# Kernel tuning notes

Hardware: AMD Instinct MI355X
Metric: run time of the kernel (lower is better)

The kernel has to match this reference:

```python
import jax, jax.numpy as jnp
import numpy as np
from jax import lax

B, C, L = 32, 64, 16384
C_OUT = 64


def conv1d(x, w, b):
    # x: [B,C,L], w: [Cout,Cin,K], b: [Cout]
    y = lax.conv_general_dilated(x, w, window_strides=(1,), padding='VALID',
                                 dimension_numbers=('NCH', 'OIH', 'NCH'))
    return y + b[None, :, None]


def setup_inputs() -> dict:
    key = jax.random.key(0)
    k1, k2, k3, k4, k5 = jax.random.split(key, 5)
    x = jax.random.normal(k1, (B, C, L), dtype=jnp.float32)
    # kernel_size = 1 (see shape_source); PyTorch Conv1d default init scale ~ 1/sqrt(Cin*K)
    s = 1.0 / np.sqrt(C * 1)
    offset_w = jax.random.uniform(k2, (C * 1, C, 1), jnp.float32, -s, s)
    offset_b = jax.random.uniform(k3, (C * 1,), jnp.float32, -s, s)
    regular_w = jax.random.uniform(k4, (C_OUT, C, 1), jnp.float32, -s, s)
    regular_b = jax.random.uniform(k5, (C_OUT,), jnp.float32, -s, s)
    return {'x': x, 'offset_w': offset_w, 'offset_b': offset_b,
            'regular_w': regular_w, 'regular_b': regular_b}


def reference(x, offset_w, offset_b, regular_w, regular_b):
    Bx, Cx, Lx = x.shape
    offsets = conv1d(x, offset_w, offset_b)                 # [B,C,L]
    base = jnp.arange(Lx, dtype=x.dtype)[None, None, :]      # [1,1,L]
    indices = jnp.clip(base + offsets, 0.0, Lx - 1)          # [B,C,L] float positions
    idx_floor = jnp.floor(indices)
    idx_ceil = jnp.ceil(indices)
    x_floor = jnp.take_along_axis(x, idx_floor.astype(jnp.int32), axis=2)
    x_ceil = jnp.take_along_axis(x, idx_ceil.astype(jnp.int32), axis=2)
    frac = indices - idx_floor
    x_deform = (1.0 - frac) * x_floor + frac * x_ceil        # [B,C,L]
    return conv1d(x_deform, regular_w, regular_b)            # [B,Cout,L]
```

## Files before the change

### kernel.cpp

```cpp
#include <hip/hip_runtime.h>


#define BDIM 256
#define BB   32
#define CC   64
#define LL   16384
#define TL   64
#define HH   8
#define ROWS (TL + 2*HH)
#define RSW  36
#define XGS  82

typedef __fp16 half_t;
typedef __attribute__((ext_vector_type(2))) __fp16 h2;
typedef __attribute__((ext_vector_type(8))) __fp16 h8;
typedef __attribute__((ext_vector_type(4))) float f4;

union H2U { h2 h; unsigned u; };
union H8U { unsigned u[4]; h8 v; };

static __device__ __forceinline__ unsigned pk(float a, float b) {
    H2U r; r.h = __builtin_amdgcn_cvt_pkrtz(a, b); return r.u;
}

static __device__ __forceinline__ void load_a_split(const float* __restrict__ wp,
                                                    int row, int ks, int q,
                                                    h8* ahi, h8* alo) {
    const float* base = wp + row * 64 + ks * 32 + q * 8;
    float4 w0 = *(const float4*)base;
    float4 w1 = *(const float4*)(base + 4);
    float v[8] = {w0.x, w0.y, w0.z, w0.w, w1.x, w1.y, w1.z, w1.w};
    H8U h, l;
    #pragma unroll
    for (int p = 0; p < 4; ++p) {
        H2U hh; hh.h = __builtin_amdgcn_cvt_pkrtz(v[2*p], v[2*p+1]);
        h.u[p] = hh.u;
        l.u[p] = pk(v[2*p] - (float)hh.h[0], v[2*p+1] - (float)hh.h[1]);
    }
    *ahi = h.v; *alo = l.v;
}

static __device__ __forceinline__ h8 load_a_f16(const float* __restrict__ wp,
                                                int row, int ks, int q) {
    const float* base = wp + row * 64 + ks * 32 + q * 8;
    float4 w0 = *(const float4*)base;
    float4 w1 = *(const float4*)(base + 4);
    float v[8] = {w0.x, w0.y, w0.z, w0.w, w1.x, w1.y, w1.z, w1.w};
    H8U r;
    #pragma unroll
    for (int p = 0; p < 4; ++p) r.u[p] = pk(v[2*p], v[2*p+1]);
    return r.v;
}

__global__ __launch_bounds__(BDIM)
void deform_conv1d_r4(const float* __restrict__ x,
                      const float* __restrict__ offw,
                      const float* __restrict__ offb,
                      const float* __restrict__ regw,
                      const float* __restrict__ regb,
                      float* __restrict__ out) {
    __shared__ __align__(16) unsigned char smem[9216 + 9216 + 10496];
    unsigned* XtH = (unsigned*)smem;
    unsigned* XtL = (unsigned*)(smem + 9216);
    half_t*   Xg  = (half_t*)(smem + 18432);
    unsigned* XdW = (unsigned*)smem;

    const int tid = threadIdx.x;
    const int bx  = blockIdx.x;
    const int lg0 = bx * TL;
    const int b   = blockIdx.y;
    const size_t xb = (size_t)b * CC * LL;

    if (bx >= 1 && bx <= (LL / TL) - 2) {
        for (int i = tid; i < 320; i += BDIM) {
            int cb = i / 20, lb = i - cb * 20;
            int c0 = cb * 4;
            int l0 = lg0 - HH + lb * 4;
            const float* pp = x + xb + (size_t)c0 * LL + l0;
            float4 v0 = *(const float4*)(pp);
            float4 v1 = *(const float4*)(pp + LL);
            float4 v2 = *(const float4*)(pp + 2 * LL);
            float4 v3 = *(const float4*)(pp + 3 * LL);
            unsigned* gw = (unsigned*)Xg;
            int wi = 41 * c0 + 2 * lb;
            gw[wi]       = pk(v0.x, v0.y); gw[wi + 1]   = pk(v0.z, v0.w);
            gw[wi + 41]  = pk(v1.x, v1.y); gw[wi + 42]  = pk(v1.z, v1.w);
            gw[wi + 82]  = pk(v2.x, v2.y); gw[wi + 83]  = pk(v2.z, v2.w);
            gw[wi + 123] = pk(v3.x, v3.y); gw[wi + 124] = pk(v3.z, v3.w);
            if (lb >= 2 && lb < 18) {
                int m = lb - 2;
                float e0[4] = {v0.x, v0.y, v0.z, v0.w};
                float e1[4] = {v1.x, v1.y, v1.z, v1.w};
                float e2[4] = {v2.x, v2.y, v2.z, v2.w};
                float e3[4] = {v3.x, v3.y, v3.z, v3.w};
                int blkw  = (cb >> 1) ^ (m & 7);
                int wbase = (4 * m) * RSW + (blkw << 2) + 2 * (cb & 1);
                #pragma unroll
                for (int rl = 0; rl < 4; ++rl) {
                    float a = e0[rl], bb = e1[rl], cc = e2[rl], dd = e3[rl];
                    H2U h0, h1;
                    h0.h = __builtin_amdgcn_cvt_pkrtz(a, bb);
                    h1.h = __builtin_amdgcn_cvt_pkrtz(cc, dd);
                    int widx = wbase + rl * RSW;
                    uint2 hw; hw.x = h0.u; hw.y = h1.u;
                    *(uint2*)&XtH[widx] = hw;
                    uint2 lw;
                    lw.x = pk(a  - (float)h0.h[0], bb - (float)h0.h[1]);
                    lw.y = pk(cc - (float)h1.h[0], dd - (float)h1.h[1]);
                    *(uint2*)&XtL[widx] = lw;
                }
            }
        }
    } else {
        for (int i = tid; i < ROWS * CC; i += BDIM) {
            int r = i >> 6, c = i & 63;
            int g = min(max(lg0 - HH + r, 0), LL - 1);
            float v = x[xb + (size_t)c * LL + g];
            H2U hv; hv.h = __builtin_amdgcn_cvt_pkrtz(v, 0.0f);
            Xg[c * XGS + r] = hv.h[0];
            int row = r - HH;
            if (row >= 0 && row < TL) {
                int blkw = (c >> 3) ^ ((row >> 2) & 7);
                int widx = row * RSW + (blkw << 2) + ((c >> 1) & 3);
                float lo = v - (float)hv.h[0];
                H2U lv; lv.h = __builtin_amdgcn_cvt_pkrtz(lo, 0.0f);
                ((half_t*)XtH)[2 * widx + (c & 1)] = hv.h[0];
                ((half_t*)XtL)[2 * widx + (c & 1)] = lv.h[0];
            }
        }
    }

    const int wv   = tid >> 6;
    const int lane = tid & 63;
    const int q    = lane >> 4;
    const int n    = lane & 15;

    h8 ahi[2], alo[2];
    load_a_split(offw, 16 * wv + n, 0, q, &ahi[0], &alo[0]);
    load_a_split(offw, 16 * wv + n, 1, q, &ahi[1], &alo[1]);
    f4 acc[4];
    {
        float4 bo = *(const float4*)(offb + 16 * wv + 4 * q);
        #pragma unroll
        for (int nt = 0; nt < 4; ++nt) acc[nt] = (f4){bo.x, bo.y, bo.z, bo.w};
    }
    __syncthreads();

    #pragma unroll
    for (int nt = 0; nt < 4; ++nt) {
        const int row = 16 * nt + n;
        const int rb  = row * RSW;
        const int sb  = (row >> 2) & 7;
        #pragma unroll
        for (int ks = 0; ks < 2; ++ks) {
            int blk = (4 * ks + q) ^ sb;
            h8 bh = *(const h8*)&XtH[rb + (blk << 2)];
            h8 bl = *(const h8*)&XtL[rb + (blk << 2)];
            acc[nt] = __builtin_amdgcn_mfma_f32_16x16x32_f16(ahi[ks], bh, acc[nt], 0, 0, 0);
            acc[nt] = __builtin_amdgcn_mfma_f32_16x16x32_f16(ahi[ks], bl, acc[nt], 0, 0, 0);
            acc[nt] = __builtin_amdgcn_mfma_f32_16x16x32_f16(alo[ks], bh, acc[nt], 0, 0, 0);
        }
    }

    #pragma unroll
    for (int nt = 0; nt < 4; ++nt) {
        const int l = lg0 + 16 * nt + n;
        #pragma unroll
        for (int reg = 0; reg < 4; ++reg) {
            const int c = 16 * wv + 4 * q + reg;
            float o  = acc[nt][reg];
            float p  = (float)l + o;
            p = __builtin_amdgcn_fmed3f(p, 0.0f, (float)(LL - 1));
            float of = floorf(p);
            float fr = p - of;
            int idx  = (int)of;
            int u    = idx - lg0 + HH;
            float x0, x1;
            if ((unsigned)u <= (unsigned)(ROWS - 2)) {
                const half_t* gp = Xg + c * XGS + u;
                x0 = (float)gp[0];
                x1 = (float)gp[1];
            } else {
                const float* xr = x + xb + (size_t)c * LL;
                x0 = xr[idx];
                x1 = xr[idx + (fr > 0.0f ? 1 : 0)];
            }
            acc[nt][reg] = x0 + fr * (x1 - x0);
        }
    }

    __syncthreads();

    #pragma unroll
    for (int nt = 0; nt < 4; ++nt) {
        const int row = 16 * nt + n;
        const int sb  = (row >> 2) & 7;
        const int bw  = (2 * wv + (q >> 1)) ^ sb;
        uint2 pw;
        pw.x = pk(acc[nt][0], acc[nt][1]);
        pw.y = pk(acc[nt][2], acc[nt][3]);
        *(uint2*)&XdW[row * RSW + (bw << 2) + 2 * (q & 1)] = pw;
    }

    h8 a2[2];
    a2[0] = load_a_f16(regw, 16 * wv + n, 0, q);
    a2[1] = load_a_f16(regw, 16 * wv + n, 1, q);
    {
        float4 br = *(const float4*)(regb + 16 * wv + 4 * q);
        #pragma unroll
        for (int nt = 0; nt < 4; ++nt) acc[nt] = (f4){br.x, br.y, br.z, br.w};
    }
    __syncthreads();

    #pragma unroll
    for (int nt = 0; nt < 4; ++nt) {
        const int row = 16 * nt + n;
        const int sb  = (row >> 2) & 7;
        #pragma unroll
        for (int ks = 0; ks < 2; ++ks) {
            int blk = (4 * ks + q) ^ sb;
            h8 bv = *(const h8*)&XdW[row * RSW + (blk << 2)];
            acc[nt] = __builtin_amdgcn_mfma_f32_16x16x32_f16(a2[ks], bv, acc[nt], 0, 0, 0);
        }
    }

    float* op = out + (size_t)b * CC * LL;
    #pragma unroll
    for (int nt = 0; nt < 4; ++nt) {
        #pragma unroll
        for (int reg = 0; reg < 4; ++reg) {
            op[(size_t)(16 * wv + 4 * q + reg) * LL + lg0 + 16 * nt + n] = acc[nt][reg];
        }
    }
}

extern "C" void kernel_launch(void* const* d_in, const int* in_sizes, int n_in,
                              void* d_out, int out_size, void* d_ws, size_t ws_size,
                              hipStream_t stream) {
    const float* x    = (const float*)d_in[0];
    const float* offw = (const float*)d_in[1];
    const float* offb = (const float*)d_in[2];
    const float* regw = (const float*)d_in[3];
    const float* regb = (const float*)d_in[4];
    float* out = (float*)d_out;

    dim3 grid(LL / TL, BB);
    deform_conv1d_r4<<<grid, dim3(BDIM), 0, stream>>>(x, offw, offb, regw, regb, out);
}
```

Before: 271.6 us.

## Merge gather tile into transposed fp16 tile, drop x-lo split and barrier

Removes the separate channel-major fp16 gather buffer and the low-part x split. One swizzled row-major fp16 tile with a halo now serves both the offset MFMA B operand and the bilinear gather, and the halo shrinks from 8 to 4. This cuts the offset GEMM from three MFMAs to two per step, reduces LDS footprint and staging stores, and removes a __syncthreads because the deformed output now goes to a separate region. In exchange, x is rounded to fp16 in the offset conv, which may hurt offset accuracy, and more gathers fall back to global memory because the halo is smaller.

```diff
diff --git a/kernel.cpp b/kernel.cpp
--- a/kernel.cpp
+++ b/kernel.cpp
@@ -6,10 +6,10 @@
 #define CC   64
 #define LL   16384
 #define TL   64
-#define HH   8
+#define HH   4
 #define ROWS (TL + 2*HH)
 #define RSW  36
-#define XGS  82
+#define RSH  72
 
 typedef __fp16 half_t;
 typedef __attribute__((ext_vector_type(2))) __fp16 h2;
@@ -53,17 +53,18 @@
 }
 
 __global__ __launch_bounds__(BDIM)
-void deform_conv1d_r4(const float* __restrict__ x,
+void deform_conv1d_r5(const float* __restrict__ x,
                       const float* __restrict__ offw,
                       const float* __restrict__ offb,
                       const float* __restrict__ regw,
                       const float* __restrict__ regb,
                       float* __restrict__ out) {
-    __shared__ __align__(16) unsigned char smem[9216 + 9216 + 10496];
+    __shared__ __align__(16) unsigned char smem[10368 + 9216];
     unsigned* XtH = (unsigned*)smem;
-    unsigned* XtL = (unsigned*)(smem + 9216);
-    half_t*   Xg  = (half_t*)(smem + 18432);
-    unsigned* XdW = (unsigned*)smem;
+    unsigned* XdW = (unsigned*)(smem + 10368);
+    half_t*   XtHh = (half_t*)smem;
+    half_t*   Xdh  = (half_t*)(smem + 10368);
+    (void)Xdh;
 
     const int tid = threadIdx.x;
     const int bx  = blockIdx.x;
@@ -72,8 +73,8 @@
     const size_t xb = (size_t)b * CC * LL;
 
     if (bx >= 1 && bx <= (LL / TL) - 2) {
-        for (int i = tid; i < 320; i += BDIM) {
-            int cb = i / 20, lb = i - cb * 20;
+        for (int i = tid; i < 288; i += BDIM) {
+            int cb = i / 18, lb = i - cb * 18;
             int c0 = cb * 4;
             int l0 = lg0 - HH + lb * 4;
             const float* pp = x + xb + (size_t)c0 * LL + l0;
@@ -81,34 +82,18 @@
             float4 v1 = *(const float4*)(pp + LL);
             float4 v2 = *(const float4*)(pp + 2 * LL);
             float4 v3 = *(const float4*)(pp + 3 * LL);
-            unsigned* gw = (unsigned*)Xg;
-            int wi = 41 * c0 + 2 * lb;
-            gw[wi]       = pk(v0.x, v0.y); gw[wi + 1]   = pk(v0.z, v0.w);
-            gw[wi + 41]  = pk(v1.x, v1.y); gw[wi + 42]  = pk(v1.z, v1.w);
-            gw[wi + 82]  = pk(v2.x, v2.y); gw[wi + 83]  = pk(v2.z, v2.w);
-            gw[wi + 123] = pk(v3.x, v3.y); gw[wi + 124] = pk(v3.z, v3.w);
-            if (lb >= 2 && lb < 18) {
-                int m = lb - 2;
-                float e0[4] = {v0.x, v0.y, v0.z, v0.w};
-                float e1[4] = {v1.x, v1.y, v1.z, v1.w};
-                float e2[4] = {v2.x, v2.y, v2.z, v2.w};
-                float e3[4] = {v3.x, v3.y, v3.z, v3.w};
-                int blkw  = (cb >> 1) ^ (m & 7);
-                int wbase = (4 * m) * RSW + (blkw << 2) + 2 * (cb & 1);
-                #pragma unroll
-                for (int rl = 0; rl < 4; ++rl) {
-                    float a = e0[rl], bb = e1[rl], cc = e2[rl], dd = e3[rl];
-                    H2U h0, h1;
-                    h0.h = __builtin_amdgcn_cvt_pkrtz(a, bb);
-                    h1.h = __builtin_amdgcn_cvt_pkrtz(cc, dd);
-                    int widx = wbase + rl * RSW;
-                    uint2 hw; hw.x = h0.u; hw.y = h1.u;
-                    *(uint2*)&XtH[widx] = hw;
-                    uint2 lw;
-                    lw.x = pk(a  - (float)h0.h[0], bb - (float)h0.h[1]);
-                    lw.y = pk(cc - (float)h1.h[0], dd - (float)h1.h[1]);
-                    *(uint2*)&XtL[widx] = lw;
-                }
+            float e0[4] = {v0.x, v0.y, v0.z, v0.w};
+            float e1[4] = {v1.x, v1.y, v1.z, v1.w};
+            float e2[4] = {v2.x, v2.y, v2.z, v2.w};
+            float e3[4] = {v3.x, v3.y, v3.z, v3.w};
+            int blkw  = (cb >> 1) ^ (lb & 7);
+            int wbase = (4 * lb) * RSW + (blkw << 2) + 2 * (cb & 1);
+            #pragma unroll
+            for (int rl = 0; rl < 4; ++rl) {
+                uint2 hw;
+                hw.x = pk(e0[rl], e1[rl]);
+                hw.y = pk(e2[rl], e3[rl]);
+                *(uint2*)&XtH[wbase + rl * RSW] = hw;
             }
         }
     } else {
@@ -116,17 +101,8 @@
             int r = i >> 6, c = i & 63;
             int g = min(max(lg0 - HH + r, 0), LL - 1);
             float v = x[xb + (size_t)c * LL + g];
-            H2U hv; hv.h = __builtin_amdgcn_cvt_pkrtz(v, 0.0f);
-            Xg[c * XGS + r] = hv.h[0];
-            int row = r - HH;
-            if (row >= 0 && row < TL) {
-                int blkw = (c >> 3) ^ ((row >> 2) & 7);
-                int widx = row * RSW + (blkw << 2) + ((c >> 1) & 3);
-                float lo = v - (float)hv.h[0];
-                H2U lv; lv.h = __builtin_amdgcn_cvt_pkrtz(lo, 0.0f);
-                ((half_t*)XtH)[2 * widx + (c & 1)] = hv.h[0];
-                ((half_t*)XtL)[2 * widx + (c & 1)] = lv.h[0];
-            }
+            int blk = (c >> 3) ^ ((r >> 2) & 7);
+            XtHh[r * RSH + (blk << 3) + (c & 7)] = (half_t)v;
         }
     }
 
@@ -148,17 +124,15 @@
 
     #pragma unroll
     for (int nt = 0; nt < 4; ++nt) {
-        const int row = 16 * nt + n;
-        const int rb  = row * RSW;
-        const int sb  = (row >> 2) & 7;
+        const int r  = 16 * nt + n + HH;
+        const int rb = r * RSW;
+        const int sb = (r >> 2) & 7;
         #pragma unroll
         for (int ks = 0; ks < 2; ++ks) {
             int blk = (4 * ks + q) ^ sb;
-            h8 bh = *(const h8*)&XtH[rb + (blk << 2)];
-            h8 bl = *(const h8*)&XtL[rb + (blk << 2)];
-            acc[nt] = __builtin_amdgcn_mfma_f32_16x16x32_f16(ahi[ks], bh, acc[nt], 0, 0, 0);
-            acc[nt] = __builtin_amdgcn_mfma_f32_16x16x32_f16(ahi[ks], bl, acc[nt], 0, 0, 0);
-            acc[nt] = __builtin_amdgcn_mfma_f32_16x16x32_f16(alo[ks], bh, acc[nt], 0, 0, 0);
+            h8 bv = *(const h8*)&XtH[rb + (blk << 2)];
+            acc[nt] = __builtin_amdgcn_mfma_f32_16x16x32_f16(ahi[ks], bv, acc[nt], 0, 0, 0);
+            acc[nt] = __builtin_amdgcn_mfma_f32_16x16x32_f16(alo[ks], bv, acc[nt], 0, 0, 0);
         }
     }
 
@@ -177,9 +151,10 @@
             int u    = idx - lg0 + HH;
             float x0, x1;
             if ((unsigned)u <= (unsigned)(ROWS - 2)) {
-                const half_t* gp = Xg + c * XGS + u;
-                x0 = (float)gp[0];
-                x1 = (float)gp[1];
+                int b0 = (c >> 3) ^ ((u >> 2) & 7);
+                int b1 = (c >> 3) ^ (((u + 1) >> 2) & 7);
+                x0 = (float)XtHh[u * RSH + (b0 << 3) + (c & 7)];
+                x1 = (float)XtHh[(u + 1) * RSH + (b1 << 3) + (c & 7)];
             } else {
                 const float* xr = x + xb + (size_t)c * LL;
                 x0 = xr[idx];
@@ -188,8 +163,6 @@
             acc[nt][reg] = x0 + fr * (x1 - x0);
         }
     }
-
-    __syncthreads();
 
     #pragma unroll
     for (int nt = 0; nt < 4; ++nt) {
@@ -245,5 +218,5 @@
     float* out = (float*)d_out;
 
     dim3 grid(LL / TL, BB);
-    deform_conv1d_r4<<<grid, dim3(BDIM), 0, stream>>>(x, offw, offb, regw, regb, out);
-}
+    deform_conv1d_r5<<<grid, dim3(BDIM), 0, stream>>>(x, offw, offb, regw, regb, out);
+}
```

New measurement: 256.8 us. -5.4%, faster.
